# Kernel optimization log

Measured on AMD Instinct MI355X. Metric: run time of the kernel, lower is better.

Reference implementation:

```python
import jax, jax.numpy as jnp
import numpy as np

B, N, IN_DIM, OUT_DIM, H = 8, 1024, 512, 512, 8
SUP = OUT_DIM // H  # support_dim per head = 64


def setup_inputs() -> dict:
    key = jax.random.key(0)
    ks = jax.random.split(key, 6)
    # 0/1 dense adjacency with self-loops so no row is fully masked
    A = jax.random.randint(ks[0], (B, N, N), 0, 2).astype(jnp.float32)
    A = jnp.maximum(A, jnp.eye(N, dtype=jnp.float32)[None])
    X = jax.random.normal(ks[1], (B, N, IN_DIM), dtype=jnp.float32)
    # parameters, uniform(-1/sqrt(fan_last), 1/sqrt(fan_last)) as in reset_parameters
    sw = 1.0 / np.sqrt(SUP)
    W = jax.random.uniform(ks[2], (H, IN_DIM, SUP), minval=-sw, maxval=sw, dtype=jnp.float32)
    w1 = jax.random.uniform(ks[3], (H, SUP), minval=-sw, maxval=sw, dtype=jnp.float32)
    w2 = jax.random.uniform(ks[4], (H, SUP), minval=-sw, maxval=sw, dtype=jnp.float32)
    b = jax.random.uniform(ks[5], (2, H), minval=-1.0, maxval=1.0, dtype=jnp.float32)
    b1, b2 = b[0], b[1]
    return {"A": A, "X": X, "W": W, "w1": w1, "b1": b1, "w2": w2, "b2": b2}


def reference(A, X, W, w1, b1, w2, b2):
    # per-head projection: [B,H,N,SUP]
    inputs = jnp.einsum('bni,hio->bhno', X, W)
    # additive attention logits: self_fc [B,H,N,1] + neigh_fc [B,H,1,N]
    self_fc = jnp.einsum('bhno,ho->bhn', inputs, w1) + b1[None, :, None]
    neigh_fc = jnp.einsum('bhno,ho->bhn', inputs, w2) + b2[None, :, None]
    logits = jax.nn.leaky_relu(self_fc[..., :, None] + neigh_fc[..., None, :], 0.01)
    mask = -1e9 * (1.0 - A)  # [B,N,N]
    alphas = jax.nn.softmax(logits + mask[:, None], axis=-1)  # [B,H,N,N]
    out = jnp.einsum('bhnm,bhmo->bhno', alphas, inputs)
    out = jax.nn.relu(out)  # default activation = torch.relu
    # concat heads on last dim (head i contiguous), matching torch.cat
    return out.transpose(0, 2, 1, 3).reshape(B, N, H * SUP)
```

## Files before the change

### kernel.cpp

```cpp
#include <hip/hip_runtime.h>
#include <hip/hip_fp16.h>

#define BB 8
#define NN 1024
#define IN_DIM 512
#define HH 8
#define SUP 64
#define HS (HH * SUP)

typedef _Float16 half8 __attribute__((ext_vector_type(8)));
typedef float floatx4 __attribute__((ext_vector_type(4)));

__global__ __launch_bounds__(256) void kprep(const float* __restrict__ A,
                                             unsigned char* __restrict__ Am,
                                             const float* __restrict__ W,
                                             _Float16* __restrict__ Wt) {
    __shared__ float tile[64][65];
    const int bid = blockIdx.x;
    const int t   = threadIdx.x;
    if (bid < 2048) {
        const int gw   = bid * 4 + (t >> 6);
        const int lane = t & 63;
        const float* arow = A + (size_t)gw * NN;
        unsigned long long keep = 0;
#pragma unroll
        for (int g = 0; g < 16; g++) {
            float a = arow[g * 64 + lane];
            unsigned long long bal = __ballot(a > 0.5f);
            if (lane == g) keep = bal;
        }
        if (lane < 16)
            *(unsigned long long*)(Am + (size_t)gw * 128 + lane * 8) = keep;
    } else {
        const int wb = bid - 2048;
        const int it = wb & 7;
        const int h  = wb >> 3;
        {
            const int i  = t >> 2;
            const int o0 = (t & 3) * 16;
            const float* src = W + ((size_t)h * IN_DIM + it * 64 + i) * SUP + o0;
#pragma unroll
            for (int j = 0; j < 4; j++) {
                float4 v = ((const float4*)src)[j];
                tile[i][o0 + j * 4 + 0] = v.x;
                tile[i][o0 + j * 4 + 1] = v.y;
                tile[i][o0 + j * 4 + 2] = v.z;
                tile[i][o0 + j * 4 + 3] = v.w;
            }
        }
        __syncthreads();
        {
            const int o  = t >> 2;
            const int i0 = (t & 3) * 16;
            _Float16 buf[16];
#pragma unroll
            for (int j = 0; j < 16; j++) buf[j] = (_Float16)tile[i0 + j][o];
            _Float16* dst = Wt + ((size_t)h * SUP + o) * IN_DIM + it * 64 + i0;
            *(half8*)dst       = *(half8*)buf;
            *(half8*)(dst + 8) = *(half8*)(buf + 8);
        }
    }
}

__global__ __launch_bounds__(256) void k1_proj(const float* __restrict__ X,
                                               const _Float16* __restrict__ Wt,
                                               const float* __restrict__ w1,
                                               const float* __restrict__ b1,
                                               const float* __restrict__ w2,
                                               const float* __restrict__ b2,
                                               _Float16* __restrict__ Pt,
                                               float* __restrict__ s_g,
                                               float* __restrict__ t_g,
                                               float* __restrict__ tmax16) {
    __shared__ __align__(16) _Float16 xs[2][64 * 40];
    __shared__ __align__(16) _Float16 wsh[2][64 * 40];
    __shared__ __align__(16) _Float16 po[64 * 72];
    __shared__ float tred[64];

    const int bh = blockIdx.y;
    const int b  = bh >> 3;
    const int h  = bh & 7;
    const int n0 = blockIdx.x * 64;
    const int t    = threadIdx.x;
    const int wave = t >> 6;
    const int lane = t & 63;
    const int quad = lane >> 4;
    const int l15  = lane & 15;
    const int row  = t >> 2;
    const int koff = (t & 3) * 8;

    floatx4 acc[4];
#pragma unroll
    for (int i = 0; i < 4; i++) acc[i] = {0.f, 0.f, 0.f, 0.f};

    float w1v[4], w2v[4];
#pragma unroll
    for (int ct = 0; ct < 4; ct++) {
        w1v[ct] = w1[h * 64 + ct * 16 + l15];
        w2v[ct] = w2[h * 64 + ct * 16 + l15];
    }
    const float b1h = b1[h];
    const float b2h = b2[h];

    const float*    xbase = X + ((size_t)b * NN + n0 + row) * IN_DIM;
    const _Float16* wbase = Wt + ((size_t)h * SUP + row) * IN_DIM;

    float4 xa = ((const float4*)(xbase + koff))[0];
    float4 xb = ((const float4*)(xbase + koff))[1];
    half8  wv = *(const half8*)(wbase + koff);

    for (int it = 0; it < 16; it++) {
        const int cur = it & 1;
        {
            _Float16 xh[8] = {(_Float16)xa.x, (_Float16)xa.y, (_Float16)xa.z, (_Float16)xa.w,
                              (_Float16)xb.x, (_Float16)xb.y, (_Float16)xb.z, (_Float16)xb.w};
            *(half8*)&xs[cur][row * 40 + koff]  = *(half8*)xh;
            *(half8*)&wsh[cur][row * 40 + koff] = wv;
        }
        __syncthreads();
        if (it < 15) {
            const float* src = xbase + (it + 1) * 32 + koff;
            xa = ((const float4*)src)[0];
            xb = ((const float4*)src)[1];
            wv = *(const half8*)(wbase + (it + 1) * 32 + koff);
        }
        half8 af = *(const half8*)&xs[cur][(wave * 16 + l15) * 40 + quad * 8];
#pragma unroll
        for (int ct = 0; ct < 4; ct++) {
            half8 bf = *(const half8*)&wsh[cur][(ct * 16 + l15) * 40 + quad * 8];
            acc[ct] = __builtin_amdgcn_mfma_f32_16x16x32_f16(af, bf, acc[ct], 0, 0, 0);
        }
    }
    __syncthreads();

#pragma unroll
    for (int ct = 0; ct < 4; ct++) {
#pragma unroll
        for (int r = 0; r < 4; r++) {
            int o = ct * 16 + l15;
            int n = wave * 16 + quad * 4 + r;
            po[o * 72 + n] = (_Float16)acc[ct][r];
        }
    }
#pragma unroll
    for (int r = 0; r < 4; r++) {
        float sp = 0.f, tp = 0.f;
#pragma unroll
        for (int ct = 0; ct < 4; ct++) {
            sp += acc[ct][r] * w1v[ct];
            tp += acc[ct][r] * w2v[ct];
        }
#pragma unroll
        for (int off = 1; off < 16; off <<= 1) {
            sp += __shfl_xor(sp, off);
            tp += __shfl_xor(tp, off);
        }
        if (l15 == 0) {
            const int n = wave * 16 + quad * 4 + r;
            s_g[(size_t)bh * NN + n0 + n] = sp + b1h;
            float tv = tp + b2h;
            t_g[(size_t)bh * NN + n0 + n] = tv;
            tred[n] = tv;
        }
    }
    __syncthreads();
    {
        const int o   = t >> 2;
        const int nof = (t & 3) * 16;
        _Float16* dst = Pt + ((size_t)bh * SUP + o) * NN + n0 + nof;
        *(half8*)dst       = *(const half8*)&po[o * 72 + nof];
        *(half8*)(dst + 8) = *(const half8*)&po[o * 72 + nof + 8];
    }
    if (t == 0) {
        float m = -1e30f;
#pragma unroll
        for (int i = 0; i < 64; i++) m = fmaxf(m, tred[i]);
        tmax16[bh * 16 + blockIdx.x] = m;
    }
}

__global__ __launch_bounds__(512) void k2_attn(const unsigned char* __restrict__ Am,
                                               const _Float16* __restrict__ Pt,
                                               const float* __restrict__ s_g,
                                               const float* __restrict__ t_g,
                                               const float* __restrict__ tmax16,
                                               float* __restrict__ out) {
    __shared__ __align__(16) _Float16 vts[2][64 * 136];
    __shared__ __align__(16) float tl[NN];

    const int bh = blockIdx.y;
    const int b  = bh >> 3;
    const int h  = bh & 7;
    const int n0 = blockIdx.x * 128;
    const int t    = threadIdx.x;
    const int wave = t >> 6;
    const int lane = t & 63;
    const int quad = lane >> 4;
    const int l15  = lane & 15;
    const int row4 = t >> 3;
    const int seg  = t & 7;

    ((float2*)tl)[t] = ((const float2*)(t_g + (size_t)bh * NN))[t];

    float tmax = -1e30f;
#pragma unroll
    for (int i = 0; i < 16; i++) tmax = fmaxf(tmax, tmax16[bh * 16 + i]);

    const int myrow = wave * 16 + l15;
    const float sv = s_g[(size_t)bh * NN + n0 + myrow];
    const float xc = sv + tmax;
    const float cv = fmaxf(xc, 0.01f * xc);

    floatx4 acc[4];
#pragma unroll
    for (int i = 0; i < 4; i++) acc[i] = {0.f, 0.f, 0.f, 0.f};
    float zp = 0.f;

    const _Float16* pb = Pt + ((size_t)bh * SUP + row4) * NN + seg * 16;
    half8 v0 = ((const half8*)pb)[0];
    half8 v1 = ((const half8*)pb)[1];
    const uint4* mrow = (const uint4*)(Am + ((size_t)b * NN + n0 + myrow) * 128);
    uint4 mcur = mrow[0];

    for (int mt = 0; mt < 8; mt++) {
        const int cur = mt & 1;
        {
            _Float16* d = &vts[cur][row4 * 136 + seg * 16];
            ((half8*)d)[0] = v0;
            ((half8*)d)[1] = v1;
        }
        __syncthreads();
        uint4 mnext;
        if (mt < 7) {
            const _Float16* p = pb + (mt + 1) * 128;
            v0 = ((const half8*)p)[0];
            v1 = ((const half8*)p)[1];
            mnext = mrow[mt + 1];
        }
        const unsigned mw[4] = {mcur.x, mcur.y, mcur.z, mcur.w};
        const int m0 = mt * 128;
#pragma unroll
        for (int kk = 0; kk < 4; kk++) {
            const unsigned mbyte = (mw[kk] >> (quad * 8)) & 0xffu;
            const int kbase = m0 + kk * 32 + quad * 8;
            float4 ta = *(const float4*)&tl[kbase];
            float4 tb = *(const float4*)&tl[kbase + 4];
            float tv[8] = {ta.x, ta.y, ta.z, ta.w, tb.x, tb.y, tb.z, tb.w};
            _Float16 wb[8];
#pragma unroll
            for (int j = 0; j < 8; j++) {
                float x = sv + tv[j];
                float l = fmaxf(x, 0.01f * x);
                float e = __expf(l - cv);
                float we = (mbyte & (1u << j)) ? e : 0.f;
                zp += we;
                wb[j] = (_Float16)we;
            }
            half8 af = *(half8*)wb;
#pragma unroll
            for (int ct = 0; ct < 4; ct++) {
                half8 bf = *(const half8*)&vts[cur][(ct * 16 + l15) * 136 + kk * 32 + quad * 8];
                acc[ct] = __builtin_amdgcn_mfma_f32_16x16x32_f16(af, bf, acc[ct], 0, 0, 0);
            }
        }
        if (mt < 7) mcur = mnext;
    }

    zp += __shfl_xor(zp, 16);
    zp += __shfl_xor(zp, 32);
    const float rzown = 1.0f / zp;

#pragma unroll
    for (int r = 0; r < 4; r++) {
        const int rr = wave * 16 + quad * 4 + r;
        const float rz = __shfl(rzown, quad * 20 + r);
#pragma unroll
        for (int ct = 0; ct < 4; ct++) {
            float v = acc[ct][r] * rz;
            v = v > 0.f ? v : 0.f;
            out[((size_t)b * NN + n0 + rr) * HS + h * SUP + ct * 16 + l15] = v;
        }
    }
}

extern "C" void kernel_launch(void* const* d_in, const int* in_sizes, int n_in,
                              void* d_out, int out_size, void* d_ws, size_t ws_size,
                              hipStream_t stream) {
    const float* A  = (const float*)d_in[0];
    const float* X  = (const float*)d_in[1];
    const float* W  = (const float*)d_in[2];
    const float* w1 = (const float*)d_in[3];
    const float* b1 = (const float*)d_in[4];
    const float* w2 = (const float*)d_in[5];
    const float* b2 = (const float*)d_in[6];
    float* out = (float*)d_out;

    char* ws = (char*)d_ws;
    _Float16*      Wt     = (_Float16*)(ws);
    _Float16*      Pt     = (_Float16*)(ws + 524288);
    float*         s_g    = (float*)(ws + 8912896);
    float*         t_g    = (float*)(ws + 9175040);
    float*         tmax16 = (float*)(ws + 9437184);
    unsigned char* Am     = (unsigned char*)(ws + 9441280);

    hipLaunchKernelGGL(kprep, dim3(2048 + 64), dim3(256), 0, stream, A, Am, W, Wt);
    hipLaunchKernelGGL(k1_proj, dim3(NN / 64, BB * HH), dim3(256), 0, stream,
                       X, Wt, w1, b1, w2, b2, Pt, s_g, t_g, tmax16);
    hipLaunchKernelGGL(k2_attn, dim3(NN / 128, BB * HH), dim3(512), 0, stream,
                       Am, Pt, s_g, t_g, tmax16, out);
}
```

Baseline: 136.7 us.

## Pre-convert X to fp16, drop LDS staging in projection, use packed fp16 softmax

Adds a pass in the prep kernel that converts X to fp16 once, so the projection kernel no longer re-reads and converts fp32 X for each of the eight heads. The projection kernel now loads MFMA fragments straight from global memory, with no LDS double-buffering or barriers. The attention kernel computes leaky-relu and exp2 with packed half2 math, masks with a bitmask lookup table and accumulates the row sum with fdot2. This trades precision, since the logits and exponentials are now in fp16 and may lose accuracy or overflow, for less ALU work in the hot loop.

```diff
diff --git a/kernel.cpp b/kernel.cpp
--- a/kernel.cpp
+++ b/kernel.cpp
@@ -9,12 +9,16 @@
 #define HS (HH * SUP)
 
 typedef _Float16 half8 __attribute__((ext_vector_type(8)));
+typedef _Float16 half4v __attribute__((ext_vector_type(4)));
+typedef _Float16 half2v __attribute__((ext_vector_type(2)));
 typedef float floatx4 __attribute__((ext_vector_type(4)));
 
 __global__ __launch_bounds__(256) void kprep(const float* __restrict__ A,
                                              unsigned char* __restrict__ Am,
                                              const float* __restrict__ W,
-                                             _Float16* __restrict__ Wt) {
+                                             _Float16* __restrict__ Wt,
+                                             const float* __restrict__ X,
+                                             _Float16* __restrict__ Xh) {
     __shared__ float tile[64][65];
     const int bid = blockIdx.x;
     const int t   = threadIdx.x;
@@ -31,7 +35,7 @@
         }
         if (lane < 16)
             *(unsigned long long*)(Am + (size_t)gw * 128 + lane * 8) = keep;
-    } else {
+    } else if (bid < 2112) {
         const int wb = bid - 2048;
         const int it = wb & 7;
         const int h  = wb >> 3;
@@ -59,10 +63,19 @@
             *(half8*)dst       = *(half8*)buf;
             *(half8*)(dst + 8) = *(half8*)(buf + 8);
         }
+    } else {
+        const int xb = bid - 2112;
+#pragma unroll 4
+        for (int i = 0; i < 32; i++) {
+            const size_t idx = (((size_t)xb * 32 + i) * 256 + t) * 4;
+            float4 v = *(const float4*)(X + idx);
+            half4v h = {(_Float16)v.x, (_Float16)v.y, (_Float16)v.z, (_Float16)v.w};
+            *(half4v*)(Xh + idx) = h;
+        }
     }
 }
 
-__global__ __launch_bounds__(256) void k1_proj(const float* __restrict__ X,
+__global__ __launch_bounds__(256) void k1_proj(const _Float16* __restrict__ Xh,
                                                const _Float16* __restrict__ Wt,
                                                const float* __restrict__ w1,
                                                const float* __restrict__ b1,
@@ -72,8 +85,6 @@
                                                float* __restrict__ s_g,
                                                float* __restrict__ t_g,
                                                float* __restrict__ tmax16) {
-    __shared__ __align__(16) _Float16 xs[2][64 * 40];
-    __shared__ __align__(16) _Float16 wsh[2][64 * 40];
     __shared__ __align__(16) _Float16 po[64 * 72];
     __shared__ float tred[64];
 
@@ -86,8 +97,6 @@
     const int lane = t & 63;
     const int quad = lane >> 4;
     const int l15  = lane & 15;
-    const int row  = t >> 2;
-    const int koff = (t & 3) * 8;
 
     floatx4 acc[4];
 #pragma unroll
@@ -102,36 +111,21 @@
     const float b1h = b1[h];
     const float b2h = b2[h];
 
-    const float*    xbase = X + ((size_t)b * NN + n0 + row) * IN_DIM;
-    const _Float16* wbase = Wt + ((size_t)h * SUP + row) * IN_DIM;
-
-    float4 xa = ((const float4*)(xbase + koff))[0];
-    float4 xb = ((const float4*)(xbase + koff))[1];
-    half8  wv = *(const half8*)(wbase + koff);
-
-    for (int it = 0; it < 16; it++) {
-        const int cur = it & 1;
-        {
-            _Float16 xh[8] = {(_Float16)xa.x, (_Float16)xa.y, (_Float16)xa.z, (_Float16)xa.w,
-                              (_Float16)xb.x, (_Float16)xb.y, (_Float16)xb.z, (_Float16)xb.w};
-            *(half8*)&xs[cur][row * 40 + koff]  = *(half8*)xh;
-            *(half8*)&wsh[cur][row * 40 + koff] = wv;
-        }
-        __syncthreads();
-        if (it < 15) {
-            const float* src = xbase + (it + 1) * 32 + koff;
-            xa = ((const float4*)src)[0];
-            xb = ((const float4*)src)[1];
-            wv = *(const half8*)(wbase + (it + 1) * 32 + koff);
-        }
-        half8 af = *(const half8*)&xs[cur][(wave * 16 + l15) * 40 + quad * 8];
-#pragma unroll
-        for (int ct = 0; ct < 4; ct++) {
-            half8 bf = *(const half8*)&wsh[cur][(ct * 16 + l15) * 40 + quad * 8];
-            acc[ct] = __builtin_amdgcn_mfma_f32_16x16x32_f16(af, bf, acc[ct], 0, 0, 0);
-        }
-    }
-    __syncthreads();
+    const _Float16* xf = Xh + ((size_t)(b * NN + n0 + wave * 16 + l15)) * IN_DIM + quad * 8;
+    const _Float16* wf = Wt + ((size_t)(h * SUP + l15)) * IN_DIM + quad * 8;
+
+#pragma unroll 4
+    for (int k0 = 0; k0 < IN_DIM; k0 += 32) {
+        half8 af  = *(const half8*)(xf + k0);
+        half8 bf0 = *(const half8*)(wf + k0);
+        half8 bf1 = *(const half8*)(wf + 16 * IN_DIM + k0);
+        half8 bf2 = *(const half8*)(wf + 32 * IN_DIM + k0);
+        half8 bf3 = *(const half8*)(wf + 48 * IN_DIM + k0);
+        acc[0] = __builtin_amdgcn_mfma_f32_16x16x32_f16(af, bf0, acc[0], 0, 0, 0);
+        acc[1] = __builtin_amdgcn_mfma_f32_16x16x32_f16(af, bf1, acc[1], 0, 0, 0);
+        acc[2] = __builtin_amdgcn_mfma_f32_16x16x32_f16(af, bf2, acc[2], 0, 0, 0);
+        acc[3] = __builtin_amdgcn_mfma_f32_16x16x32_f16(af, bf3, acc[3], 0, 0, 0);
+    }
 
 #pragma unroll
     for (int ct = 0; ct < 4; ct++) {
@@ -186,7 +180,8 @@
                                                const float* __restrict__ tmax16,
                                                float* __restrict__ out) {
     __shared__ __align__(16) _Float16 vts[2][64 * 136];
-    __shared__ __align__(16) float tl[NN];
+    __shared__ __align__(16) unsigned t2l[NN / 2];
+    __shared__ __align__(16) uint4 lutm[256];
 
     const int bh = blockIdx.y;
     const int b  = bh >> 3;
@@ -200,7 +195,20 @@
     const int row4 = t >> 3;
     const int seg  = t & 7;
 
-    ((float2*)tl)[t] = ((const float2*)(t_g + (size_t)bh * NN))[t];
+    {
+        float2 tv2 = ((const float2*)(t_g + (size_t)bh * NN))[t];
+        half2v tp = {(_Float16)tv2.x, (_Float16)tv2.y};
+        t2l[t] = *(unsigned*)&tp;
+    }
+    if (t < 256) {
+        unsigned e = (unsigned)t;
+        uint4 v;
+        v.x = ((e & 1u)   ? 0xFFFFu : 0u) | ((e & 2u)   ? 0xFFFF0000u : 0u);
+        v.y = ((e & 4u)   ? 0xFFFFu : 0u) | ((e & 8u)   ? 0xFFFF0000u : 0u);
+        v.z = ((e & 16u)  ? 0xFFFFu : 0u) | ((e & 32u)  ? 0xFFFF0000u : 0u);
+        v.w = ((e & 64u)  ? 0xFFFFu : 0u) | ((e & 128u) ? 0xFFFF0000u : 0u);
+        lutm[t] = v;
+    }
 
     float tmax = -1e30f;
 #pragma unroll
@@ -210,6 +218,14 @@
     const float sv = s_g[(size_t)bh * NN + n0 + myrow];
     const float xc = sv + tmax;
     const float cv = fmaxf(xc, 0.01f * xc);
+    const float l2e = 1.44269504f;
+    const _Float16 sc1h = (_Float16)((sv - cv) * l2e);
+    const _Float16 sc2h = (_Float16)(-0.99f * cv * l2e);
+    const half2v sc1 = {sc1h, sc1h};
+    const half2v sc2 = {sc2h, sc2h};
+    const half2v vl2e = {(_Float16)l2e, (_Float16)l2e};
+    const half2v v001 = {(_Float16)0.01f, (_Float16)0.01f};
+    const half2v ones2 = {(_Float16)1.0f, (_Float16)1.0f};
 
     floatx4 acc[4];
 #pragma unroll
@@ -238,25 +254,31 @@
             mnext = mrow[mt + 1];
         }
         const unsigned mw[4] = {mcur.x, mcur.y, mcur.z, mcur.w};
-        const int m0 = mt * 128;
 #pragma unroll
         for (int kk = 0; kk < 4; kk++) {
             const unsigned mbyte = (mw[kk] >> (quad * 8)) & 0xffu;
-            const int kbase = m0 + kk * 32 + quad * 8;
-            float4 ta = *(const float4*)&tl[kbase];
-            float4 tb = *(const float4*)&tl[kbase + 4];
-            float tv[8] = {ta.x, ta.y, ta.z, ta.w, tb.x, tb.y, tb.z, tb.w};
-            _Float16 wb[8];
-#pragma unroll
-            for (int j = 0; j < 8; j++) {
-                float x = sv + tv[j];
-                float l = fmaxf(x, 0.01f * x);
-                float e = __expf(l - cv);
-                float we = (mbyte & (1u << j)) ? e : 0.f;
-                zp += we;
-                wb[j] = (_Float16)we;
+            uint4 mx = lutm[mbyte];
+            const unsigned mxw[4] = {mx.x, mx.y, mx.z, mx.w};
+            uint4 tw = *(const uint4*)&t2l[mt * 64 + kk * 16 + quad * 4];
+            union { uint4 u; half2v h[4]; } tt; tt.u = tw;
+            union { half2v h[4]; half8 h8; } wbu;
+#pragma unroll
+            for (int p = 0; p < 4; p++) {
+                half2v y = tt.h[p] * vl2e + sc1;
+                half2v w = y * v001 + sc2;
+                half2v z = __builtin_elementwise_max(y, w);
+                __half2 zz = *(__half2*)&z;
+                __half2 ee = h2exp2(zz);
+                unsigned eb = (*(unsigned*)&ee) & mxw[p];
+                half2v e2 = *(half2v*)&eb;
+#if __has_builtin(__builtin_amdgcn_fdot2)
+                zp = __builtin_amdgcn_fdot2(e2, ones2, zp, false);
+#else
+                zp += (float)e2.x + (float)e2.y;
+#endif
+                wbu.h[p] = e2;
             }
-            half8 af = *(half8*)wb;
+            half8 af = wbu.h8;
 #pragma unroll
             for (int ct = 0; ct < 4; ct++) {
                 half8 bf = *(const half8*)&vts[cur][(ct * 16 + l15) * 136 + kk * 32 + quad * 8];
@@ -302,10 +324,11 @@
     float*         t_g    = (float*)(ws + 9175040);
     float*         tmax16 = (float*)(ws + 9437184);
     unsigned char* Am     = (unsigned char*)(ws + 9441280);
-
-    hipLaunchKernelGGL(kprep, dim3(2048 + 64), dim3(256), 0, stream, A, Am, W, Wt);
+    _Float16*      Xh     = (_Float16*)(ws + 10489856);
+
+    hipLaunchKernelGGL(kprep, dim3(2048 + 64 + 128), dim3(256), 0, stream, A, Am, W, Wt, X, Xh);
     hipLaunchKernelGGL(k1_proj, dim3(NN / 64, BB * HH), dim3(256), 0, stream,
-                       X, Wt, w1, b1, w2, b2, Pt, s_g, t_g, tmax16);
+                       Xh, Wt, w1, b1, w2, b2, Pt, s_g, t_g, tmax16);
     hipLaunchKernelGGL(k2_attn, dim3(NN / 128, BB * HH), dim3(512), 0, stream,
                        Am, Pt, s_g, t_g, tmax16, out);
 }
```

Measured after the change: 159.6 us. 1.17x slower.
